# Kernel tuning notes

Measured on AMD Instinct MI355X. Metric: run time of the kernel, lower is better.

The kernel has to match this reference:

```python
import jax, jax.numpy as jnp
import numpy as np

B, S, D = 2, 2048, 4096
H, KV, HD = 32, 8, 128
THETA = 10000.0


def rotate_half(x):
    x1, x2 = x[..., : HD // 2], x[..., HD // 2 :]
    return jnp.concatenate((-x2, x1), axis=-1)


def setup_inputs() -> dict:
    key = jax.random.key(0)
    ks = jax.random.split(key, 8)
    s = 1.0 / np.sqrt(D)
    return {
        "hidden_states": jax.random.normal(ks[0], (B, S, D), jnp.float32),
        "modality_indicators": jax.random.randint(ks[1], (B, S), 0, 2, jnp.int64 if jax.config.jax_enable_x64 else jnp.int32),
        "position_ids": jnp.arange(S, dtype=jnp.int32),
        "Wq": jax.random.normal(ks[2], (D, H * HD), jnp.float32) * s,
        "Wk0": jax.random.normal(ks[3], (D, KV * HD), jnp.float32) * s,
        "Wk1": jax.random.normal(ks[4], (D, KV * HD), jnp.float32) * s,
        "Wv0": jax.random.normal(ks[5], (D, KV * HD), jnp.float32) * s,
        "Wv1": jax.random.normal(ks[6], (D, KV * HD), jnp.float32) * s,
        "Wo": jax.random.normal(ks[7], (H * HD, D), jnp.float32) * s,
    }


def reference(hidden_states, modality_indicators, position_ids, Wq, Wk0, Wk1, Wv0, Wv1, Wo):
    x = hidden_states
    # Multiway (modality-routed) k/v projections: per-token select between two linears.
    sel = (modality_indicators == 1)[..., None]  # [B,S,1]
    q = x @ Wq                                   # [B,S,H*HD]
    k = jnp.where(sel, x @ Wk1, x @ Wk0)         # [B,S,KV*HD]
    v = jnp.where(sel, x @ Wv1, x @ Wv0)

    q = q.reshape(B, S, H, HD).transpose(0, 2, 1, 3)    # [B,H,S,HD]
    k = k.reshape(B, S, KV, HD).transpose(0, 2, 1, 3)   # [B,KV,S,HD]
    v = v.reshape(B, S, KV, HD).transpose(0, 2, 1, 3)

    # RoPE cache and application (emb = cat(freqs, freqs))
    inv_freq = 1.0 / (THETA ** (jnp.arange(0, HD, 2, dtype=jnp.float32) / HD))
    freqs = position_ids.astype(jnp.float32)[:, None] * inv_freq[None, :]   # [S,HD/2]
    emb = jnp.concatenate((freqs, freqs), axis=-1)                          # [S,HD]
    cos = jnp.cos(emb)[None, None, :, :]                                    # [1,1,S,HD]
    sin = jnp.sin(emb)[None, None, :, :]
    q = q * cos + rotate_half(q) * sin
    k = k * cos + rotate_half(k) * sin

    # GQA: repeat kv heads
    n_rep = H // KV
    k = jnp.repeat(k, n_rep, axis=1)  # [B,H,S,HD]
    v = jnp.repeat(v, n_rep, axis=1)

    scores = jnp.einsum("bhqd,bhkd->bhqk", q, k) / np.sqrt(HD)
    causal = jnp.tril(jnp.ones((S, S), dtype=bool))
    scores = jnp.where(causal[None, None], scores, jnp.finfo(scores.dtype).min)
    attn = jax.nn.softmax(scores, axis=-1)
    ctx = jnp.einsum("bhqk,bhkd->bhqd", attn, v)            # [B,H,S,HD]
    ctx = ctx.transpose(0, 2, 1, 3).reshape(B, S, H * HD)
    return ctx @ Wo
```

## Files before the change

### kernel.cpp

```cpp
#include <hip/hip_runtime.h>

typedef unsigned short u16;
typedef unsigned int   u32;
using bf16x8 = __attribute__((ext_vector_type(8))) __bf16;
using f32x4  = __attribute__((ext_vector_type(4))) float;
using f32x16 = __attribute__((ext_vector_type(16))) float;
using u32x4  = __attribute__((ext_vector_type(4))) unsigned int;
using ushort8 = __attribute__((ext_vector_type(8))) unsigned short;


__device__ __forceinline__ u16 f2bf(float f) {
  u32 u = __builtin_bit_cast(u32, f);
  return (u16)((u + 0x7fffu + ((u >> 16) & 1u)) >> 16);
}
__device__ __forceinline__ float bf2f(u16 h) {
  return __builtin_bit_cast(float, (u32)h << 16);
}
__device__ __forceinline__ f32x4 mfma16(bf16x8 a, bf16x8 b, f32x4 c) {
  return __builtin_amdgcn_mfma_f32_16x16x32_bf16(a, b, c, 0, 0, 0);
}
__device__ __forceinline__ f32x16 mfma32(bf16x8 a, bf16x8 b, f32x16 c) {
  return __builtin_amdgcn_mfma_f32_32x32x16_bf16(a, b, c, 0, 0, 0);
}
__device__ __forceinline__ f32x16 zero16() {
  f32x16 z;
#pragma unroll
  for (int i = 0; i < 16; ++i) z[i] = 0.f;
  return z;
}
__device__ __forceinline__ void g2l16(const void* gp, void* lp) {
  __builtin_amdgcn_global_load_lds(
      (__attribute__((address_space(1))) void*)(void*)gp,
      (__attribute__((address_space(3))) void*)lp, 16, 0, 0);
}

__global__ void k_cvt(const float* __restrict__ in, u16* __restrict__ out, int n4) {
  int i = blockIdx.x * 256 + threadIdx.x;
  if (i >= n4) return;
  float4 v = ((const float4*)in)[i];
  ushort4 o;
  o.x = f2bf(v.x); o.y = f2bf(v.y); o.z = f2bf(v.z); o.w = f2bf(v.w);
  ((ushort4*)out)[i] = o;
}

__device__ __forceinline__ void tcvt_tile(const float* __restrict__ in, u16* __restrict__ out,
                                          int K, int N, int nt, int kt, u16 (*t)[72]) {
  const int n0 = nt * 64, k0 = kt * 64;
  const int tid = threadIdx.x;
  const int r = tid >> 2, c4 = (tid & 3) * 16;
  const float* src = in + (size_t)(k0 + r) * N + n0 + c4;
#pragma unroll
  for (int q = 0; q < 4; ++q) {
    float4 v = *(const float4*)(src + 4 * q);
    t[c4 + 4 * q + 0][r] = f2bf(v.x);
    t[c4 + 4 * q + 1][r] = f2bf(v.y);
    t[c4 + 4 * q + 2][r] = f2bf(v.z);
    t[c4 + 4 * q + 3][r] = f2bf(v.w);
  }
  __syncthreads();
  u16* dst = out + (size_t)(n0 + r) * K + k0 + c4;
#pragma unroll
  for (int hh = 0; hh < 2; ++hh)
    *(ushort8*)(dst + 8 * hh) = *(const ushort8*)(&t[r][c4 + 8 * hh]);
}

__global__ __launch_bounds__(256) void k_tcvt(const float* __restrict__ in, u16* __restrict__ out,
                                              int K, int N) {
  __shared__ u16 t[64][72];
  tcvt_tile(in, out, K, N, blockIdx.x, blockIdx.y, t);
}

__global__ __launch_bounds__(256) void k_tcvt5(const float* __restrict__ Wq, const float* __restrict__ Wk0,
                                               const float* __restrict__ Wv0, const float* __restrict__ Wk1,
                                               const float* __restrict__ Wv1, u16* __restrict__ WqT,
                                               u16* __restrict__ Wkv0T, u16* __restrict__ Wkv1T) {
  __shared__ u16 t[64][72];
  int bid = blockIdx.x;
  if (bid < 4096) {
    tcvt_tile(Wq, WqT, 4096, 4096, bid & 63, bid >> 6, t);
  } else {
    int r = bid - 4096;
    int mat = r >> 10, rr = r & 1023;
    const float* src = (mat == 0) ? Wk0 : (mat == 1) ? Wv0 : (mat == 2) ? Wk1 : Wv1;
    u16* dst = (mat == 0) ? Wkv0T : (mat == 1) ? (Wkv0T + (size_t)1024 * 4096)
                                  : (mat == 2) ? Wkv1T : (Wkv1T + (size_t)1024 * 4096);
    tcvt_tile(src, dst, 4096, 1024, rr & 15, rr >> 4, t);
  }
}

__global__ void k_scan(const int* __restrict__ mod, int* __restrict__ perm, int* __restrict__ meta) {
  __shared__ int ps[1024];
  const int b = blockIdx.x, t = threadIdx.x;
  perm[b * 2304 + t] = -1;
  perm[b * 2304 + 1024 + t] = -1;
  if (t < 256) perm[b * 2304 + 2048 + t] = -1;
  const int i0 = 2 * t, i1 = 2 * t + 1;
  const int f0 = (mod[b * 2048 + i0] != 1) ? 1 : 0;
  const int f1 = (mod[b * 2048 + i1] != 1) ? 1 : 0;
  const int sum = f0 + f1;
  ps[t] = sum;
  __syncthreads();
  for (int off = 1; off < 1024; off <<= 1) {
    int v = (t >= off) ? ps[t - off] : 0;
    __syncthreads();
    ps[t] += v;
    __syncthreads();
  }
  const int total0 = ps[1023];
  const int excl = ps[t] - sum;
  const int nt0 = (total0 + 255) >> 8;
  const int off1 = nt0 * 256;
  const int s0 = f0 ? excl : off1 + (i0 - excl);
  const int s1 = f1 ? (excl + f0) : off1 + (i1 - (excl + f0));
  perm[b * 2304 + s0] = i0;
  perm[b * 2304 + s1] = i1;
  if (t == 0) { meta[b * 2] = total0; meta[b * 2 + 1] = nt0; }
}

#define BARSB() { __builtin_amdgcn_s_barrier(); __builtin_amdgcn_sched_barrier(0); }
#define VMC(N)  asm volatile("s_waitcnt vmcnt(" #N ")" ::: "memory")

#define READ_A(MH, SL) { _Pragma("unroll") for (int mf_ = 0; mf_ < 4; ++mf_) {       \
    const char* a_ = (const char*)lds8 + (SL)*65536 + (MH)*16384 + (arow + mf_*16)*128; \
    afr[mf_][0] = *(const bf16x8*)(a_ + swc0);                                        \
    afr[mf_][1] = *(const bf16x8*)(a_ + swc1); } }

#define READ_B(NH, SL) { _Pragma("unroll") for (int nf_ = 0; nf_ < 2; ++nf_) {       \
    const char* b_ = (const char*)lds8 + (SL)*65536 + 32768 + (NH)*16384 + (brow + nf_*16)*128; \
    bfr[nf_][0] = *(const bf16x8*)(b_ + swc0);                                        \
    bfr[nf_][1] = *(const bf16x8*)(b_ + swc1); } }

#define MM16(MH, NH) { __builtin_amdgcn_s_setprio(1);                                 \
  _Pragma("unroll") for (int mf_ = 0; mf_ < 4; ++mf_)                                 \
    _Pragma("unroll") for (int nf_ = 0; nf_ < 2; ++nf_) {                             \
      acc[MH][mf_][NH][nf_] = mfma16(afr[mf_][0], bfr[nf_][0], acc[MH][mf_][NH][nf_]); \
      acc[MH][mf_][NH][nf_] = mfma16(afr[mf_][1], bfr[nf_][1], acc[MH][mf_][NH][nf_]); } \
  __builtin_amdgcn_s_setprio(0); }

#define STAGE_A(T, MH) { int ts_ = (T) < 64 ? (T) : 63;                               \
    char* d_ = (char*)lds8 + ((T)&1)*65536 + (MH)*16384 + wid*1024;                   \
    g2l16(pA0[MH] + ts_*64, d_); g2l16(pA1[MH] + ts_*64, d_ + 8192); }

#define STAGE_B(T, NH) { int ts_ = (T) < 64 ? (T) : 63;                               \
    char* d_ = (char*)lds8 + ((T)&1)*65536 + 32768 + (NH)*16384 + wid*1024;           \
    g2l16(pB0[NH] + ts_*64, d_); g2l16(pB1[NH] + ts_*64, d_ + 8192); }

#define G8_MAINLOOP()                                                                 \
  STAGE_A(0,0); STAGE_B(0,1); STAGE_A(0,1); STAGE_B(0,0);                             \
  STAGE_A(1,0); STAGE_B(1,1); STAGE_A(1,1);                                           \
  VMC(6); BARSB();                                                                    \
  for (int i_ = 0; i_ < 32; ++i_) {                                                   \
    const int ta_ = 2 * i_;                                                           \
    READ_A(0,0); READ_B(0,0); STAGE_B(ta_+1, 0); BARSB(); MM16(0,0); BARSB();         \
    READ_B(1,0);              STAGE_A(ta_+2, 0); BARSB(); MM16(0,1); BARSB();         \
    READ_A(1,0);              STAGE_B(ta_+2, 1); BARSB(); MM16(1,1); BARSB();         \
    READ_B(0,0);              STAGE_A(ta_+2, 1); BARSB(); MM16(1,0); VMC(4); BARSB(); \
    READ_A(0,1); READ_B(0,1); STAGE_B(ta_+2, 0); BARSB(); MM16(0,0); BARSB();         \
    READ_B(1,1);              STAGE_A(ta_+3, 0); BARSB(); MM16(0,1); BARSB();         \
    READ_A(1,1);              STAGE_B(ta_+3, 1); BARSB(); MM16(1,1); BARSB();         \
    READ_B(0,1);              STAGE_A(ta_+3, 1); BARSB(); MM16(1,0); VMC(4); BARSB(); \
  }

__global__ __launch_bounds__(512, 2) void k_gemm8(const u16* __restrict__ A, const u16* __restrict__ Bt,
                                                  float* __restrict__ Cp) {
  __shared__ u16 lds8[65536];
  const int tid = threadIdx.x, wid = tid >> 6, l = tid & 63, g = l >> 4, li = l & 15;
  const int wr = wid >> 2, wc = wid & 3;
  const int bid = blockIdx.x;
  const int swz = (bid & 7) * 32 + (bid >> 3);
  const int m0 = (swz >> 4) * 256, n0 = (swz & 15) * 256;

  const int swc0 = (g * 16) ^ ((li & 7) << 4);
  const int swc1 = (64 + g * 16) ^ ((li & 7) << 4);
  const int arow = wr * 64 + li;
  const int brow = wc * 32 + li;

  const int l8a = tid * 16, l8b = 8192 + tid * 16;
  const int oa = l8a ^ (((l8a >> 7) & 7) << 4), ob = l8b ^ (((l8b >> 7) & 7) << 4);
  const int rl0 = oa >> 7, cb0 = oa & 127, rl1 = ob >> 7, cb1 = ob & 127;
  const int RA0 = (rl0 >> 6) * 128 + (rl0 & 63), RA1 = (rl1 >> 6) * 128 + (rl1 & 63);
  const int CB0 = (rl0 >> 5) * 64 + (rl0 & 31), CB1 = (rl1 >> 5) * 64 + (rl1 & 31);
  const u16 *pA0[2], *pA1[2], *pB0[2], *pB1[2];
#pragma unroll
  for (int mh = 0; mh < 2; ++mh) {
    pA0[mh] = A + (size_t)(m0 + RA0 + mh * 64) * 4096 + cb0 / 2;
    pA1[mh] = A + (size_t)(m0 + RA1 + mh * 64) * 4096 + cb1 / 2;
    pB0[mh] = Bt + (size_t)(n0 + CB0 + mh * 32) * 4096 + cb0 / 2;
    pB1[mh] = Bt + (size_t)(n0 + CB1 + mh * 32) * 4096 + cb1 / 2;
  }

  bf16x8 afr[4][2], bfr[2][2];
  const f32x4 vzero = {0.f, 0.f, 0.f, 0.f};
  f32x4 acc[2][4][2][2];
#pragma unroll
  for (int a = 0; a < 2; ++a)
#pragma unroll
    for (int b = 0; b < 4; ++b)
#pragma unroll
      for (int c = 0; c < 2; ++c)
#pragma unroll
        for (int d = 0; d < 2; ++d) acc[a][b][c][d] = vzero;

  G8_MAINLOOP();

#pragma unroll
  for (int mh = 0; mh < 2; ++mh)
#pragma unroll
    for (int mf = 0; mf < 4; ++mf)
#pragma unroll
      for (int nh = 0; nh < 2; ++nh)
#pragma unroll
        for (int nf = 0; nf < 2; ++nf)
#pragma unroll
          for (int j = 0; j < 4; ++j) {
            int row = m0 + wr * 128 + mh * 64 + mf * 16 + g * 4 + j;
            int col = n0 + wc * 64 + nh * 32 + nf * 16 + li;
            Cp[(size_t)row * 4096 + col] = acc[mh][mf][nh][nf][j];
          }
}

__global__ __launch_bounds__(512, 2) void k_gemmQKV(const u16* __restrict__ Xb, const u16* __restrict__ WqT,
                                                    const u16* __restrict__ B0, const u16* __restrict__ B1,
                                                    const int* __restrict__ perm, const int* __restrict__ meta,
                                                    u16* __restrict__ Qr, u16* __restrict__ Ksel,
                                                    u16* __restrict__ Vsel) {
  __shared__ u16 lds8[65536];
  const int tid = threadIdx.x, wid = tid >> 6, l = tid & 63, g = l >> 4, li = l & 15;
  const int wr = wid >> 2, wc = wid & 3;
  const int bid = blockIdx.x;
  const bool isQ = bid < 256;

  const int swc0 = (g * 16) ^ ((li & 7) << 4);
  const int swc1 = (64 + g * 16) ^ ((li & 7) << 4);
  const int arow = wr * 64 + li;
  const int brow = wc * 32 + li;

  const int l8a = tid * 16, l8b = 8192 + tid * 16;
  const int oa = l8a ^ (((l8a >> 7) & 7) << 4), ob = l8b ^ (((l8b >> 7) & 7) << 4);
  const int rl0 = oa >> 7, cb0 = oa & 127, rl1 = ob >> 7, cb1 = ob & 127;
  const int RA0 = (rl0 >> 6) * 128 + (rl0 & 63), RA1 = (rl1 >> 6) * 128 + (rl1 & 63);
  const int CB0 = (rl0 >> 5) * 64 + (rl0 & 31), CB1 = (rl1 >> 5) * 64 + (rl1 & 31);

  int m0 = 0, n0 = 0, bb = 0, tm = 0;
  const u16 *pA0[2], *pA1[2], *pB0[2], *pB1[2];
  if (isQ) {
    const int swz = (bid & 7) * 32 + (bid >> 3);
    m0 = (swz >> 4) * 256; n0 = (swz & 15) * 256;
#pragma unroll
    for (int mh = 0; mh < 2; ++mh) {
      pA0[mh] = Xb + (size_t)(m0 + RA0 + mh * 64) * 4096 + cb0 / 2;
      pA1[mh] = Xb + (size_t)(m0 + RA1 + mh * 64) * 4096 + cb1 / 2;
      pB0[mh] = WqT + (size_t)(n0 + CB0 + mh * 32) * 4096 + cb0 / 2;
      pB1[mh] = WqT + (size_t)(n0 + CB1 + mh * 32) * 4096 + cb1 / 2;
    }
  } else {
    const int kb = bid - 256;
    const int seg = kb >> 3;
    n0 = (kb & 7) * 256;
    bb = seg / 9; tm = seg % 9;
    const int nt0 = meta[bb * 2 + 1];
    const u16* Bt = (tm >= nt0) ? B1 : B0;
    const int pbase = bb * 2304 + tm * 256;
#pragma unroll
    for (int mh = 0; mh < 2; ++mh) {
      int t0 = perm[pbase + RA0 + mh * 64]; if (t0 < 0) t0 = 0;
      int t1 = perm[pbase + RA1 + mh * 64]; if (t1 < 0) t1 = 0;
      pA0[mh] = Xb + ((size_t)bb * 2048 + t0) * 4096 + cb0 / 2;
      pA1[mh] = Xb + ((size_t)bb * 2048 + t1) * 4096 + cb1 / 2;
      pB0[mh] = Bt + (size_t)(n0 + CB0 + mh * 32) * 4096 + cb0 / 2;
      pB1[mh] = Bt + (size_t)(n0 + CB1 + mh * 32) * 4096 + cb1 / 2;
    }
  }

  bf16x8 afr[4][2], bfr[2][2];
  const f32x4 vzero = {0.f, 0.f, 0.f, 0.f};
  f32x4 acc[2][4][2][2];
#pragma unroll
  for (int a = 0; a < 2; ++a)
#pragma unroll
    for (int b = 0; b < 4; ++b)
#pragma unroll
      for (int c = 0; c < 2; ++c)
#pragma unroll
        for (int d = 0; d < 2; ++d) acc[a][b][c][d] = vzero;

  G8_MAINLOOP();

  if (isQ) {
#pragma unroll
    for (int mh = 0; mh < 2; ++mh)
#pragma unroll
      for (int mf = 0; mf < 4; ++mf)
#pragma unroll
        for (int nh = 0; nh < 2; ++nh)
#pragma unroll
          for (int nf = 0; nf < 2; ++nf)
#pragma unroll
            for (int j = 0; j < 4; ++j) {
              int row = m0 + wr * 128 + mh * 64 + mf * 16 + g * 4 + j;
              int col = n0 + wc * 64 + nh * 32 + nf * 16 + li;
              int b = row >> 11, s = row & 2047, h = col >> 7, d = col & 127;
              Qr[(((size_t)(b * 32 + h)) * 2048 + s) * 128 + d] = f2bf(acc[mh][mf][nh][nf][j]);
            }
  } else {
#pragma unroll
    for (int mh = 0; mh < 2; ++mh)
#pragma unroll
      for (int mf = 0; mf < 4; ++mf)
#pragma unroll
        for (int nh = 0; nh < 2; ++nh)
#pragma unroll
          for (int nf = 0; nf < 2; ++nf)
#pragma unroll
            for (int j = 0; j < 4; ++j) {
              int slot = tm * 256 + wr * 128 + mh * 64 + mf * 16 + g * 4 + j;
              int tok = perm[bb * 2304 + slot];
              if (tok >= 0) {
                int col = n0 + wc * 64 + nh * 32 + nf * 16 + li;
                int kv = col >> 10, hh = (col >> 7) & 7, d = col & 127;
                u16* dst = (kv ? Vsel : Ksel) + (((size_t)(bb * 8 + hh)) * 2048 + tok) * 128 + d;
                *dst = f2bf(acc[mh][mf][nh][nf][j]);
              }
            }
  }
}

__global__ __launch_bounds__(256) void k_ropekv(u16* __restrict__ Q, const u16* __restrict__ Ks,
                                                const u16* __restrict__ Vs, const int* __restrict__ pos,
                                                u16* __restrict__ Kr, u16* __restrict__ Vt) {
  __shared__ u16 Vl[64][136];
  const int bid = blockIdx.x;
  const int tid = threadIdx.x, l = tid & 63;
  const float invf = expf((float)l * -0.14391156831212787f);
  if (bid < 32768) {
    int row = bid * 4 + (tid >> 6);
    int s = row & 2047;
    u16* p = Q + (size_t)row * 128;
    float x1 = bf2f(p[l]), x2 = bf2f(p[l + 64]);
    float ang = (float)pos[s] * invf;
    float cs = cosf(ang), sn = sinf(ang);
    const float sc = 0.08838834764831845f;
    p[l] = f2bf((x1 * cs - x2 * sn) * sc);
    p[l + 64] = f2bf((x2 * cs + x1 * sn) * sc);
  } else {
    int blk = bid - 32768;
    int st = blk & 31, kvh = (blk >> 5) & 7, b = blk >> 8;
    int s0 = st * 64;
    int wid = tid >> 6;
    size_t slab = (size_t)(b * 8 + kvh) * 2048;
    for (int rr = 0; rr < 16; ++rr) {
      int r = wid * 16 + rr;
      int s = s0 + r;
      const u16* ks = Ks + (slab + s) * 128;
      const u16* vs = Vs + (slab + s) * 128;
      float ang = (float)pos[s] * invf;
      float cs = cosf(ang), sn = sinf(ang);
      float x1 = bf2f(ks[l]), x2 = bf2f(ks[l + 64]);
      u16* kd = Kr + (slab + s) * 128;
      kd[l] = f2bf(x1 * cs - x2 * sn);
      kd[l + 64] = f2bf(x2 * cs + x1 * sn);
      Vl[r][l] = vs[l];
      Vl[r][l + 64] = vs[l + 64];
    }
    __syncthreads();
    int d = tid >> 1, si0 = (tid & 1) * 32;
    u16* vd = Vt + ((size_t)(b * 8 + kvh) * 128 + d) * 2048 + s0 + si0;
#pragma unroll
    for (int k4 = 0; k4 < 8; ++k4) {
      ushort4 o;
      o.x = Vl[si0 + k4 * 4 + 0][d];
      o.y = Vl[si0 + k4 * 4 + 1][d];
      o.z = Vl[si0 + k4 * 4 + 2][d];
      o.w = Vl[si0 + k4 * 4 + 3][d];
      *(ushort4*)(vd + k4 * 4) = o;
    }
  }
}

__global__ __launch_bounds__(256, 2) void k_attn(const u16* __restrict__ Q, const u16* __restrict__ Kr,
                                                 const u16* __restrict__ Vt, u16* __restrict__ ctx) {
  __shared__ u16 Kl[2 * 64 * 128];
  __shared__ u16 Vl[2 * 128 * 64];
  const int id = blockIdx.x;
  const int gkv = id & 15, j = id >> 4;
  const int b = gkv >> 3, kvh = gkv & 7;
  const int h = kvh * 4 + (j & 3);
  const int p = j >> 2;
  const int bh = b * 32 + h;
  const int tid = threadIdx.x, w = tid >> 6, l = tid & 63;
  const int lo5 = l & 31, hi = l >> 5;
  const bool hib = hi != 0;
  const size_t kvslab = (size_t)(b * 8 + kvh) * 2048;
  const u16* Kg = Kr + kvslab * 128;
  const u16* Vg = Vt + kvslab * 128;
  const float L2E = 1.4426950408889634f;

  auto stage = [&](int kt, int bi) {
#pragma unroll
    for (int i = 0; i < 4; ++i) {
      int c = w * 4 + i;
      int slot = c * 1024 + l * 16;
      {
        int row = slot >> 8;
        int inner = (slot & 255) ^ ((row & 15) << 4);
        g2l16((const char*)Kg + kt * 16384 + row * 256 + inner,
              (char*)Kl + bi * 16384 + c * 1024);
      }
      {
        int row = slot >> 7;
        int inner = (slot & 127) ^ ((row & 7) << 4);
        g2l16((const char*)Vg + (size_t)row * 4096 + kt * 128 + inner,
              (char*)Vl + bi * 16384 + c * 1024);
      }
    }
  };

  for (int hf = 0; hf < 2; ++hf) {
    const int qi = hf ? (15 - p) : p;
    const int q0 = qi * 128;
    const int qlane = q0 + w * 32 + lo5;
    const u16* qrow = Q + ((size_t)bh * 2048 + qlane) * 128;
    bf16x8 qf[8];
#pragma unroll
    for (int kk = 0; kk < 8; ++kk) qf[kk] = *(const bf16x8*)(qrow + kk * 16 + hi * 8);

    f32x16 ot[4];
#pragma unroll
    for (int i = 0; i < 4; ++i) ot[i] = zero16();
    float m = -1e30f, ls = 0.f;

    const int nkt = 2 * qi + 2;
    stage(0, 0);
    stage(1, 1);
    for (int kt = 0; kt < nkt; ++kt) {
      if (kt + 1 < nkt) {
        asm volatile("s_waitcnt vmcnt(8)" ::: "memory");
      } else {
        asm volatile("s_waitcnt vmcnt(0)" ::: "memory");
      }
      __builtin_amdgcn_s_barrier();
      __builtin_amdgcn_sched_barrier(0);
      const char* kbase = (const char*)Kl + (kt & 1) * 16384;
      const char* vbase = (const char*)Vl + (kt & 1) * 16384;
      const int ktb = kt * 64;
      if (ktb <= q0 + w * 32 + 31) {
        f32x16 st[2];
        st[0] = zero16(); st[1] = zero16();
#pragma unroll
        for (int kk = 0; kk < 8; ++kk) {
          bf16x8 kfr[2];
#pragma unroll
          for (int mf = 0; mf < 2; ++mf) {
            int row = mf * 32 + lo5;
            kfr[mf] = *(const bf16x8*)(kbase + row * 256 + ((kk * 32 + hi * 16) ^ ((row & 15) << 4)));
          }
          __builtin_amdgcn_s_setprio(1);
          st[0] = mfma32(kfr[0], qf[kk], st[0]);
          st[1] = mfma32(kfr[1], qf[kk], st[1]);
          __builtin_amdgcn_s_setprio(0);
        }
        if (ktb + 63 > q0 + w * 32) {
#pragma unroll
          for (int mf = 0; mf < 2; ++mf)
#pragma unroll
            for (int r = 0; r < 16; ++r) {
              int kg = ktb + mf * 32 + (r & 3) + 8 * (r >> 2) + 4 * hi;
              if (kg > qlane) st[mf][r] = -3.0e38f;
            }
        }
        float t[16];
#pragma unroll
        for (int r = 0; r < 16; ++r) t[r] = fmaxf(st[0][r], st[1][r]);
#pragma unroll
        for (int s = 8; s >= 1; s >>= 1)
#pragma unroll
          for (int r = 0; r < s; ++r) t[r] = fmaxf(t[r], t[r + s]);
        float pmax = fmaxf(t[0], __shfl_xor(t[0], 32));
        if (!__all(pmax <= m + 8.f)) {
          float nm = fmaxf(m, pmax);
          float resc = exp2f((m - nm) * L2E);
          m = nm;
          ls *= resc;
#pragma unroll
          for (int i = 0; i < 4; ++i)
#pragma unroll
            for (int r = 0; r < 16; ++r) ot[i][r] *= resc;
        }
#pragma unroll
        for (int mf = 0; mf < 2; ++mf)
#pragma unroll
          for (int r = 0; r < 16; ++r) st[mf][r] = exp2f((st[mf][r] - m) * L2E);
        float u[16];
#pragma unroll
        for (int r = 0; r < 16; ++r) u[r] = st[0][r] + st[1][r];
#pragma unroll
        for (int s = 8; s >= 1; s >>= 1)
#pragma unroll
          for (int r = 0; r < s; ++r) u[r] += u[r + s];
        ls += u[0] + __shfl_xor(u[0], 32);
        u32 pkv[16];
#pragma unroll
        for (int mf = 0; mf < 2; ++mf)
#pragma unroll
          for (int tt = 0; tt < 8; ++tt) {
            u32 r;
            asm("v_cvt_pk_bf16_f32 %0, %1, %2" : "=v"(r) : "v"(st[mf][2 * tt]), "v"(st[mf][2 * tt + 1]));
            pkv[mf * 8 + tt] = r;
          }
        bf16x8 pfrag[4];
#pragma unroll
        for (int kk = 0; kk < 4; ++kk) {
          int c = (kk >> 1) * 8 + (kk & 1) * 4;
          u32 m0 = hib ? pkv[c + 2] : pkv[c + 0];
          u32 m1 = hib ? pkv[c + 3] : pkv[c + 1];
          u32 s0 = hib ? pkv[c + 0] : pkv[c + 2];
          u32 s1 = hib ? pkv[c + 1] : pkv[c + 3];
          u32 r0 = (u32)__shfl_xor((int)s0, 32);
          u32 r1 = (u32)__shfl_xor((int)s1, 32);
          u32x4 wv = {hib ? r0 : m0, hib ? r1 : m1, hib ? m0 : r0, hib ? m1 : r1};
          pfrag[kk] = __builtin_bit_cast(bf16x8, wv);
        }
#pragma unroll
        for (int mfV = 0; mfV < 4; ++mfV) {
          int row = mfV * 32 + lo5;
          const char* vb = vbase + row * 128;
          int sw = (row & 7) << 4;
          bf16x8 vf[4];
#pragma unroll
          for (int kk = 0; kk < 4; ++kk)
            vf[kk] = *(const bf16x8*)(vb + ((kk * 32 + hi * 16) ^ sw));
          __builtin_amdgcn_s_setprio(1);
#pragma unroll
          for (int kk = 0; kk < 4; ++kk) ot[mfV] = mfma32(vf[kk], pfrag[kk], ot[mfV]);
          __builtin_amdgcn_s_setprio(0);
        }
      }
      __builtin_amdgcn_s_barrier();
      if (kt + 2 < nkt) stage(kt + 2, kt & 1);
    }
    float inv = 1.0f / ls;
    u16* crow = ctx + ((size_t)(b * 2048) + qlane) * 4096 + h * 128;
#pragma unroll
    for (int mfV = 0; mfV < 4; ++mfV)
#pragma unroll
      for (int rq = 0; rq < 4; ++rq) {
        ushort4 o4;
        o4.x = f2bf(ot[mfV][rq * 4 + 0] * inv);
        o4.y = f2bf(ot[mfV][rq * 4 + 1] * inv);
        o4.z = f2bf(ot[mfV][rq * 4 + 2] * inv);
        o4.w = f2bf(ot[mfV][rq * 4 + 3] * inv);
        *(ushort4*)(crow + mfV * 32 + rq * 8 + hi * 4) = o4;
      }
  }
}

extern "C" void kernel_launch(void* const* d_in, const int* in_sizes, int n_in,
                              void* d_out, int out_size, void* d_ws, size_t ws_size,
                              hipStream_t stream) {
  (void)in_sizes; (void)n_in; (void)out_size; (void)ws_size;
  const float* X   = (const float*)d_in[0];
  const int*   mod = (const int*)d_in[1];
  const int*   pos = (const int*)d_in[2];
  const float* Wq  = (const float*)d_in[3];
  const float* Wk0 = (const float*)d_in[4];
  const float* Wk1 = (const float*)d_in[5];
  const float* Wv0 = (const float*)d_in[6];
  const float* Wv1 = (const float*)d_in[7];
  const float* Wo  = (const float*)d_in[8];
  float* out = (float*)d_out;

  u16* p = (u16*)d_ws;
  auto take = [&](size_t n) { u16* r = p; p += n; return r; };
  u16* Xb    = take(16777216);
  u16* WqT   = take(16777216);
  u16* WoT   = take(16777216);
  u16* Wkv0T = take(8388608);
  u16* Wkv1T = take(8388608);
  u16* Qr    = take(16777216);
  u16* Ksel  = take(4194304);
  u16* Vsel  = take(4194304);
  int* perm  = (int*)take(9216);
  int* meta  = (int*)take(64);
  u16* Kr  = WqT;
  u16* Vtr = WqT + 4194304;
  u16* ctx = Xb;

  k_cvt<<<dim3(16384), 256, 0, stream>>>(X, Xb, 4194304);
  k_scan<<<dim3(2), 1024, 0, stream>>>(mod, perm, meta);
  k_tcvt5<<<dim3(8192), 256, 0, stream>>>(Wq, Wk0, Wv0, Wk1, Wv1, WqT, Wkv0T, Wkv1T);

  k_gemmQKV<<<dim3(400), 512, 0, stream>>>(Xb, WqT, Wkv0T, Wkv1T, perm, meta, Qr, Ksel, Vsel);

  k_ropekv<<<dim3(33280), 256, 0, stream>>>(Qr, Ksel, Vsel, pos, Kr, Vtr);

  k_attn<<<dim3(512), 256, 0, stream>>>(Qr, Kr, Vtr, ctx);

  k_tcvt<<<dim3(64, 64), 256, 0, stream>>>(Wo, WoT, 4096, 4096);

  k_gemm8<<<dim3(256), 512, 0, stream>>>(ctx, WoT, out);
}
```

Before: 530.5 us.

## Rewrite QKV GEMM mainloop with 1024-thread blocks and 4-stage K-pipeline

The fused QKV projection GEMM moves from 512 threads with a shared G8 mainloop to 1024 threads (16 waves). Each wave now owns a 64x64 sub-tile, and K advances in 32-wide steps through a four-buffer LDS ring that prefetches three stages ahead, using direct global-to-LDS loads. It also adds priority raising around the MFMA block and a new XOR swizzle. The aim is better latency hiding and more waves in flight. The cost is a barrier on every one of 128 K-steps and a higher register and scheduling burden.

```diff
diff --git a/kernel.cpp b/kernel.cpp
--- a/kernel.cpp
+++ b/kernel.cpp
@@ -219,40 +219,57 @@
           }
 }
 
-__global__ __launch_bounds__(512, 2) void k_gemmQKV(const u16* __restrict__ Xb, const u16* __restrict__ WqT,
-                                                    const u16* __restrict__ B0, const u16* __restrict__ B1,
-                                                    const int* __restrict__ perm, const int* __restrict__ meta,
-                                                    u16* __restrict__ Qr, u16* __restrict__ Ksel,
-                                                    u16* __restrict__ Vsel) {
-  __shared__ u16 lds8[65536];
+#define TB16(T, VMLIT, DOSTAGE)                                              \
+  {                                                                          \
+    asm volatile("s_waitcnt vmcnt(" VMLIT ")" ::: "memory");                 \
+    __builtin_amdgcn_s_barrier();                                            \
+    __builtin_amdgcn_sched_barrier(0);                                       \
+    const u16* base_ = lds + ((T) & 3) * 16384;                              \
+    bf16x8 bfr[4], afr[4];                                                   \
+    _Pragma("unroll")                                                        \
+    for (int nf = 0; nf < 4; ++nf)                                           \
+      bfr[nf] = *(const bf16x8*)(base_ + boff + nf * 512);                   \
+    _Pragma("unroll")                                                        \
+    for (int mf = 0; mf < 4; ++mf)                                           \
+      afr[mf] = *(const bf16x8*)(base_ + aoff + mf * 512);                   \
+    if (DOSTAGE) stage((T) + 3);                                             \
+    __builtin_amdgcn_s_setprio(1);                                           \
+    _Pragma("unroll")                                                        \
+    for (int mf = 0; mf < 4; ++mf)                                           \
+      _Pragma("unroll")                                                      \
+      for (int nf = 0; nf < 4; ++nf)                                         \
+        acc[mf][nf] = mfma16(afr[mf], bfr[nf], acc[mf][nf]);                 \
+    __builtin_amdgcn_s_setprio(0);                                           \
+  }
+
+#define LOOP16()                                                             \
+  stage(0); stage(1); stage(2);                                              \
+  for (int t = 0; t < 125; ++t) TB16(t, "4", true);                          \
+  TB16(125, "4", false);                                                     \
+  TB16(126, "2", false);                                                     \
+  TB16(127, "0", false);
+
+__global__ __launch_bounds__(1024, 4) void k_gemmQKV(const u16* __restrict__ Xb, const u16* __restrict__ WqT,
+                                                     const u16* __restrict__ B0, const u16* __restrict__ B1,
+                                                     const int* __restrict__ perm, const int* __restrict__ meta,
+                                                     u16* __restrict__ Qr, u16* __restrict__ Ksel,
+                                                     u16* __restrict__ Vsel) {
+  __shared__ u16 lds[4 * 16384];
   const int tid = threadIdx.x, wid = tid >> 6, l = tid & 63, g = l >> 4, li = l & 15;
   const int wr = wid >> 2, wc = wid & 3;
   const int bid = blockIdx.x;
   const bool isQ = bid < 256;
 
-  const int swc0 = (g * 16) ^ ((li & 7) << 4);
-  const int swc1 = (64 + g * 16) ^ ((li & 7) << 4);
-  const int arow = wr * 64 + li;
-  const int brow = wc * 32 + li;
-
-  const int l8a = tid * 16, l8b = 8192 + tid * 16;
-  const int oa = l8a ^ (((l8a >> 7) & 7) << 4), ob = l8b ^ (((l8b >> 7) & 7) << 4);
-  const int rl0 = oa >> 7, cb0 = oa & 127, rl1 = ob >> 7, cb1 = ob & 127;
-  const int RA0 = (rl0 >> 6) * 128 + (rl0 & 63), RA1 = (rl1 >> 6) * 128 + (rl1 & 63);
-  const int CB0 = (rl0 >> 5) * 64 + (rl0 & 31), CB1 = (rl1 >> 5) * 64 + (rl1 & 31);
+  const int srow = wid * 16 + (l >> 2);
+  const int sgg = (l & 3) ^ ((l >> 3) & 3);
 
   int m0 = 0, n0 = 0, bb = 0, tm = 0;
-  const u16 *pA0[2], *pA1[2], *pB0[2], *pB1[2];
+  const u16 *pA, *pB;
   if (isQ) {
     const int swz = (bid & 7) * 32 + (bid >> 3);
     m0 = (swz >> 4) * 256; n0 = (swz & 15) * 256;
-#pragma unroll
-    for (int mh = 0; mh < 2; ++mh) {
-      pA0[mh] = Xb + (size_t)(m0 + RA0 + mh * 64) * 4096 + cb0 / 2;
-      pA1[mh] = Xb + (size_t)(m0 + RA1 + mh * 64) * 4096 + cb1 / 2;
-      pB0[mh] = WqT + (size_t)(n0 + CB0 + mh * 32) * 4096 + cb0 / 2;
-      pB1[mh] = WqT + (size_t)(n0 + CB1 + mh * 32) * 4096 + cb1 / 2;
-    }
+    pA = Xb + (size_t)(m0 + srow) * 4096 + sgg * 8;
+    pB = WqT + (size_t)(n0 + srow) * 4096 + sgg * 8;
   } else {
     const int kb = bid - 256;
     const int seg = kb >> 3;
@@ -260,68 +277,59 @@
     bb = seg / 9; tm = seg % 9;
     const int nt0 = meta[bb * 2 + 1];
     const u16* Bt = (tm >= nt0) ? B1 : B0;
-    const int pbase = bb * 2304 + tm * 256;
-#pragma unroll
-    for (int mh = 0; mh < 2; ++mh) {
-      int t0 = perm[pbase + RA0 + mh * 64]; if (t0 < 0) t0 = 0;
-      int t1 = perm[pbase + RA1 + mh * 64]; if (t1 < 0) t1 = 0;
-      pA0[mh] = Xb + ((size_t)bb * 2048 + t0) * 4096 + cb0 / 2;
-      pA1[mh] = Xb + ((size_t)bb * 2048 + t1) * 4096 + cb1 / 2;
-      pB0[mh] = Bt + (size_t)(n0 + CB0 + mh * 32) * 4096 + cb0 / 2;
-      pB1[mh] = Bt + (size_t)(n0 + CB1 + mh * 32) * 4096 + cb1 / 2;
-    }
-  }
-
-  bf16x8 afr[4][2], bfr[2][2];
+    int t0 = perm[bb * 2304 + tm * 256 + srow];
+    if (t0 < 0) t0 = 0;
+    pA = Xb + ((size_t)bb * 2048 + t0) * 4096 + sgg * 8;
+    pB = Bt + (size_t)(n0 + srow) * 4096 + sgg * 8;
+  }
+
+  auto stage = [&](int t) {
+    u16* da = (u16*)lds + (t & 3) * 16384 + wid * 512;
+    g2l16(pA + t * 32, da);
+    g2l16(pB + t * 32, da + 8192);
+  };
+
+  const int lsl8 = (g ^ ((li >> 1) & 3)) * 8;
+  const int aoff = (wr * 64 + li) * 32 + lsl8;
+  const int boff = 8192 + (wc * 64 + li) * 32 + lsl8;
+
   const f32x4 vzero = {0.f, 0.f, 0.f, 0.f};
-  f32x4 acc[2][4][2][2];
-#pragma unroll
-  for (int a = 0; a < 2; ++a)
-#pragma unroll
-    for (int b = 0; b < 4; ++b)
-#pragma unroll
-      for (int c = 0; c < 2; ++c)
-#pragma unroll
-        for (int d = 0; d < 2; ++d) acc[a][b][c][d] = vzero;
-
-  G8_MAINLOOP();
+  f32x4 acc[4][4];
+#pragma unroll
+  for (int m = 0; m < 4; ++m)
+#pragma unroll
+    for (int n = 0; n < 4; ++n) acc[m][n] = vzero;
+
+  LOOP16();
 
   if (isQ) {
 #pragma unroll
-    for (int mh = 0; mh < 2; ++mh)
-#pragma unroll
-      for (int mf = 0; mf < 4; ++mf)
-#pragma unroll
-        for (int nh = 0; nh < 2; ++nh)
-#pragma unroll
-          for (int nf = 0; nf < 2; ++nf)
-#pragma unroll
-            for (int j = 0; j < 4; ++j) {
-              int row = m0 + wr * 128 + mh * 64 + mf * 16 + g * 4 + j;
-              int col = n0 + wc * 64 + nh * 32 + nf * 16 + li;
-              int b = row >> 11, s = row & 2047, h = col >> 7, d = col & 127;
-              Qr[(((size_t)(b * 32 + h)) * 2048 + s) * 128 + d] = f2bf(acc[mh][mf][nh][nf][j]);
-            }
+    for (int mf = 0; mf < 4; ++mf)
+#pragma unroll
+      for (int nf = 0; nf < 4; ++nf)
+#pragma unroll
+        for (int j = 0; j < 4; ++j) {
+          int row = m0 + wr * 64 + mf * 16 + g * 4 + j;
+          int col = n0 + wc * 64 + nf * 16 + li;
+          int b = row >> 11, s = row & 2047, h = col >> 7, d = col & 127;
+          Qr[(((size_t)(b * 32 + h)) * 2048 + s) * 128 + d] = f2bf(acc[mf][nf][j]);
+        }
   } else {
 #pragma unroll
-    for (int mh = 0; mh < 2; ++mh)
-#pragma unroll
-      for (int mf = 0; mf < 4; ++mf)
-#pragma unroll
-        for (int nh = 0; nh < 2; ++nh)
-#pragma unroll
-          for (int nf = 0; nf < 2; ++nf)
-#pragma unroll
-            for (int j = 0; j < 4; ++j) {
-              int slot = tm * 256 + wr * 128 + mh * 64 + mf * 16 + g * 4 + j;
-              int tok = perm[bb * 2304 + slot];
-              if (tok >= 0) {
-                int col = n0 + wc * 64 + nh * 32 + nf * 16 + li;
-                int kv = col >> 10, hh = (col >> 7) & 7, d = col & 127;
-                u16* dst = (kv ? Vsel : Ksel) + (((size_t)(bb * 8 + hh)) * 2048 + tok) * 128 + d;
-                *dst = f2bf(acc[mh][mf][nh][nf][j]);
-              }
-            }
+    for (int mf = 0; mf < 4; ++mf)
+#pragma unroll
+      for (int nf = 0; nf < 4; ++nf)
+#pragma unroll
+        for (int j = 0; j < 4; ++j) {
+          int slot = tm * 256 + wr * 64 + mf * 16 + g * 4 + j;
+          int tok = perm[bb * 2304 + slot];
+          if (tok >= 0) {
+            int col = n0 + wc * 64 + nf * 16 + li;
+            int kv = col >> 10, hh = (col >> 7) & 7, d = col & 127;
+            u16* dst = (kv ? Vsel : Ksel) + (((size_t)(bb * 8 + hh)) * 2048 + tok) * 128 + d;
+            *dst = f2bf(acc[mf][nf][j]);
+          }
+        }
   }
 }
 
@@ -589,7 +597,7 @@
   k_scan<<<dim3(2), 1024, 0, stream>>>(mod, perm, meta);
   k_tcvt5<<<dim3(8192), 256, 0, stream>>>(Wq, Wk0, Wv0, Wk1, Wv1, WqT, Wkv0T, Wkv1T);
 
-  k_gemmQKV<<<dim3(400), 512, 0, stream>>>(Xb, WqT, Wkv0T, Wkv1T, perm, meta, Qr, Ksel, Vsel);
+  k_gemmQKV<<<dim3(400), 1024, 0, stream>>>(Xb, WqT, Wkv0T, Wkv1T, perm, meta, Qr, Ksel, Vsel);
 
   k_ropekv<<<dim3(33280), 256, 0, stream>>>(Qr, Ksel, Vsel, pos, Kr, Vtr);
 
```

After: 540.5 us. No clear change (+1.9%).
